# Kernel tuning notes

Measured on AMD Instinct MI355X. Metric: run time of the kernel, lower is better.

Reference implementation:

```python
import jax, jax.numpy as jnp
import numpy as np

MAX_DISP = 4  # matches init_kwargs


def setup_inputs() -> dict:
    key = jax.random.key(0)
    k1, k2 = jax.random.split(key)
    x_1 = jax.random.normal(k1, (8, 64, 256, 256), dtype=jnp.float32)
    x_2 = jax.random.normal(k2, (8, 64, 256, 256), dtype=jnp.float32)
    return {"x_1": x_1, "x_2": x_2}


def reference(x_1, x_2):
    md = MAX_DISP
    B, C, H, W = x_1.shape
    # zero-pad x_2 spatially by max_disp on all sides
    x2p = jnp.pad(x_2, ((0, 0), (0, 0), (md, md), (md, md)))
    D = 2 * md + 1
    # row-major over (dx, dy), matching torch.meshgrid(indexing='ij')
    outs = [
        jnp.mean(x_1 * jax.lax.dynamic_slice(x2p, (0, 0, dx, dy), (B, C, H, W)),
                 axis=1, keepdims=True)
        for dx in range(D) for dy in range(D)
    ]
    return jnp.concatenate(outs, axis=1)  # [B, D*D, H, W]
```

## Files before the change

### kernel.cpp

```cpp
#include <hip/hip_runtime.h>


namespace {
constexpr int kB = 8;
constexpr int kC = 64;
constexpr int kH = 256;
constexpr int kW = 256;
constexpr int kD = 9;
constexpr int kMD = 4;
}

__global__ __launch_bounds__(64) void corr_kernel(
    const float* __restrict__ x1, const float* __restrict__ x2,
    float* __restrict__ out) {
  const int bx = blockIdx.x;
  const int dx = bx % kD;
  const int h  = (bx / kD) % kH;
  const int b  = bx / (kD * kH);
  const int row = h + dx - kMD;
  const int w0  = (int)threadIdx.x * 4;

  float acc[kD][4];
#pragma unroll
  for (int dy = 0; dy < kD; ++dy)
#pragma unroll
    for (int j = 0; j < 4; ++j) acc[dy][j] = 0.0f;

  if (row >= 0 && row < kH) {
    const float* p1 = x1 + ((size_t)(b * kC) * kH + h) * kW + w0;
    const float* p2 = x2 + ((size_t)(b * kC) * kH + row) * kW + w0;
    const bool hasL = (w0 >= 4);
    const bool hasR = (w0 + 7 < kW);
    for (int c = 0; c < kC; ++c) {
      const float4 a  = *reinterpret_cast<const float4*>(p1);
      const float4 tB = *reinterpret_cast<const float4*>(p2);
      float4 tA = make_float4(0.f, 0.f, 0.f, 0.f);
      float4 tC = make_float4(0.f, 0.f, 0.f, 0.f);
      if (hasL) tA = *reinterpret_cast<const float4*>(p2 - 4);
      if (hasR) tC = *reinterpret_cast<const float4*>(p2 + 4);

      const float av[4] = {a.x, a.y, a.z, a.w};
      const float t[12] = {tA.x, tA.y, tA.z, tA.w,
                           tB.x, tB.y, tB.z, tB.w,
                           tC.x, tC.y, tC.z, tC.w};
#pragma unroll
      for (int dy = 0; dy < kD; ++dy)
#pragma unroll
        for (int j = 0; j < 4; ++j)
          acc[dy][j] = fmaf(av[j], t[dy + j], acc[dy][j]);

      p1 += kH * kW;
      p2 += kH * kW;
    }
  }

  const float inv = 1.0f / (float)kC;
  float* po = out + (((size_t)b * (kD * kD) + dx * kD) * kH + h) * kW + w0;
#pragma unroll
  for (int dy = 0; dy < kD; ++dy) {
    float4 o = make_float4(acc[dy][0] * inv, acc[dy][1] * inv,
                           acc[dy][2] * inv, acc[dy][3] * inv);
    *reinterpret_cast<float4*>(po) = o;
    po += (size_t)kH * kW;
  }
}

extern "C" void kernel_launch(void* const* d_in, const int* in_sizes, int n_in,
                              void* d_out, int out_size, void* d_ws, size_t ws_size,
                              hipStream_t stream) {
  const float* x1 = (const float*)d_in[0];
  const float* x2 = (const float*)d_in[1];
  float* out = (float*)d_out;
  const int grid = kB * kH * kD;
  corr_kernel<<<grid, 64, 0, stream>>>(x1, x2, out);
}
```

Measured before the change: 225.4 us.

## Stage row pairs in double-buffered LDS and share x2 rows across displacements

Each block now handles two output rows for all nine vertical displacements. Per channel it stages 2 x1 rows and 10 x2 rows into a swizzled, double-buffered shared-memory tile, with the next channel's global loads overlapped against compute. This replaces the old scheme, where every (row, dx) block re-read x1 and x2 from global memory. Each thread computes 8 output columns instead of 4 to raise register reuse. The cost is a barrier per channel, a 24KB LDS footprint, 72 accumulators per thread, and a much smaller grid of 1024 blocks.

```diff
diff --git a/kernel.cpp b/kernel.cpp
--- a/kernel.cpp
+++ b/kernel.cpp
@@ -7,60 +7,132 @@
 constexpr int kH = 256;
 constexpr int kW = 256;
 constexpr int kD = 9;
-constexpr int kMD = 4;
+constexpr int kCS = kH * kW;
+constexpr int kRows = 12;
+constexpr int kBufDw = kRows * kW;
 }
 
-__global__ __launch_bounds__(64) void corr_kernel(
+__device__ __forceinline__ int swz(int b) { return b ^ ((b >> 3) & 7); }
+
+__global__ __launch_bounds__(576) void corr_kernel(
     const float* __restrict__ x1, const float* __restrict__ x2,
     float* __restrict__ out) {
-  const int bx = blockIdx.x;
-  const int dx = bx % kD;
-  const int h  = (bx / kD) % kH;
-  const int b  = bx / (kD * kH);
-  const int row = h + dx - kMD;
-  const int w0  = (int)threadIdx.x * 4;
+  __shared__ float lds[2 * kBufDw];
 
-  float acc[kD][4];
+  const int bb = blockIdx.x & 7;
+  const int hp = blockIdx.x >> 3;
+  const int tid = (int)threadIdx.x;
+  const int wv = tid >> 6;
+  const int lane = tid & 63;
+  const int half = lane >> 5;
+  const int lh = lane & 31;
+  const int h = 2 * hp + half;
+  const int w0 = lh * 8;
+
+  const bool hasL = (lh > 0);
+  const bool hasR = (lh < 31);
+  const float4 z = make_float4(0.f, 0.f, 0.f, 0.f);
+
+  const size_t chanBase = (size_t)(bb * kC) * kH;
+
+  const int r0s = tid >> 6, b0s = tid & 63;
+  const float* src0;
+  bool v0;
+  if (r0s < 2) {
+    v0 = true;
+    src0 = x1 + (chanBase + (size_t)(2 * hp + r0s)) * kW + b0s * 4;
+  } else {
+    const int rr = 2 * hp + r0s - 6;
+    v0 = (rr >= 0 && rr < kH);
+    src0 = x2 + (chanBase + (size_t)(v0 ? rr : 0)) * kW + b0s * 4;
+  }
+  const int w0i = r0s * kW + swz(b0s) * 4;
+
+  const bool have1 = (tid < 192);
+  const int r1s = (576 + tid) >> 6, b1s = (576 + tid) & 63;
+  const float* src1 = x2;
+  bool v1 = false;
+  int w1i = 0;
+  if (have1) {
+    const int rr = 2 * hp + r1s - 6;
+    v1 = (rr >= 0 && rr < kH);
+    src1 = x2 + (chanBase + (size_t)(v1 ? rr : 0)) * kW + b1s * 4;
+    w1i = r1s * kW + swz(b1s) * 4;
+  }
+
+  const int a0i = half * kW + swz(2 * lh) * 4;
+  const int a1i = half * kW + swz(2 * lh + 1) * 4;
+  const int Rr = (2 + half + wv) * kW;
+  const int t0i = Rr + swz((2 * lh - 1) & 63) * 4;
+  const int t1i = Rr + swz(2 * lh) * 4;
+  const int t2i = Rr + swz(2 * lh + 1) * 4;
+  const int t3i = Rr + swz((2 * lh + 2) & 63) * 4;
+
+  float acc[kD][8];
 #pragma unroll
   for (int dy = 0; dy < kD; ++dy)
 #pragma unroll
-    for (int j = 0; j < 4; ++j) acc[dy][j] = 0.0f;
+    for (int j = 0; j < 8; ++j) acc[dy][j] = 0.0f;
 
-  if (row >= 0 && row < kH) {
-    const float* p1 = x1 + ((size_t)(b * kC) * kH + h) * kW + w0;
-    const float* p2 = x2 + ((size_t)(b * kC) * kH + row) * kW + w0;
-    const bool hasL = (w0 >= 4);
-    const bool hasR = (w0 + 7 < kW);
-    for (int c = 0; c < kC; ++c) {
-      const float4 a  = *reinterpret_cast<const float4*>(p1);
-      const float4 tB = *reinterpret_cast<const float4*>(p2);
-      float4 tA = make_float4(0.f, 0.f, 0.f, 0.f);
-      float4 tC = make_float4(0.f, 0.f, 0.f, 0.f);
-      if (hasL) tA = *reinterpret_cast<const float4*>(p2 - 4);
-      if (hasR) tC = *reinterpret_cast<const float4*>(p2 + 4);
+  {
+    const float4 g0 = v0 ? *reinterpret_cast<const float4*>(src0) : z;
+    *reinterpret_cast<float4*>(&lds[w0i]) = g0;
+    if (have1) {
+      const float4 g1 = v1 ? *reinterpret_cast<const float4*>(src1) : z;
+      *reinterpret_cast<float4*>(&lds[w1i]) = g1;
+    }
+    src0 += kCS;
+    src1 += kCS;
+  }
+  __syncthreads();
 
-      const float av[4] = {a.x, a.y, a.z, a.w};
-      const float t[12] = {tA.x, tA.y, tA.z, tA.w,
-                           tB.x, tB.y, tB.z, tB.w,
-                           tC.x, tC.y, tC.z, tC.w};
+#pragma unroll 2
+  for (int c = 0; c < kC; ++c) {
+    const int bo = (c & 1) ? kBufDw : 0;
+    const int bo2 = (c & 1) ? 0 : kBufDw;
+    const bool more = (c + 1 < kC);
+
+    float4 n0 = z, n1 = z;
+    if (more) {
+      n0 = v0 ? *reinterpret_cast<const float4*>(src0) : z;
+      if (have1) n1 = v1 ? *reinterpret_cast<const float4*>(src1) : z;
+      src0 += kCS;
+      src1 += kCS;
+    }
+
+    const float4 A0 = *reinterpret_cast<const float4*>(&lds[bo + a0i]);
+    const float4 A1 = *reinterpret_cast<const float4*>(&lds[bo + a1i]);
+    const float4 T0 = hasL ? *reinterpret_cast<const float4*>(&lds[bo + t0i]) : z;
+    const float4 T1 = *reinterpret_cast<const float4*>(&lds[bo + t1i]);
+    const float4 T2 = *reinterpret_cast<const float4*>(&lds[bo + t2i]);
+    const float4 T3 = hasR ? *reinterpret_cast<const float4*>(&lds[bo + t3i]) : z;
+
+    const float av[8] = {A0.x, A0.y, A0.z, A0.w, A1.x, A1.y, A1.z, A1.w};
+    const float t[16] = {T0.x, T0.y, T0.z, T0.w, T1.x, T1.y, T1.z, T1.w,
+                         T2.x, T2.y, T2.z, T2.w, T3.x, T3.y, T3.z, T3.w};
 #pragma unroll
-      for (int dy = 0; dy < kD; ++dy)
+    for (int dy = 0; dy < kD; ++dy)
 #pragma unroll
-        for (int j = 0; j < 4; ++j)
-          acc[dy][j] = fmaf(av[j], t[dy + j], acc[dy][j]);
+      for (int j = 0; j < 8; ++j)
+        acc[dy][j] = fmaf(av[j], t[dy + j], acc[dy][j]);
 
-      p1 += kH * kW;
-      p2 += kH * kW;
+    if (more) {
+      *reinterpret_cast<float4*>(&lds[bo2 + w0i]) = n0;
+      if (have1) *reinterpret_cast<float4*>(&lds[bo2 + w1i]) = n1;
+      __syncthreads();
     }
   }
 
   const float inv = 1.0f / (float)kC;
-  float* po = out + (((size_t)b * (kD * kD) + dx * kD) * kH + h) * kW + w0;
+  float* po = out + (((size_t)bb * (kD * kD) + wv * kD) * kH + h) * kW + w0;
 #pragma unroll
   for (int dy = 0; dy < kD; ++dy) {
-    float4 o = make_float4(acc[dy][0] * inv, acc[dy][1] * inv,
-                           acc[dy][2] * inv, acc[dy][3] * inv);
-    *reinterpret_cast<float4*>(po) = o;
+    const float4 o0 = make_float4(acc[dy][0] * inv, acc[dy][1] * inv,
+                                  acc[dy][2] * inv, acc[dy][3] * inv);
+    const float4 o1 = make_float4(acc[dy][4] * inv, acc[dy][5] * inv,
+                                  acc[dy][6] * inv, acc[dy][7] * inv);
+    *reinterpret_cast<float4*>(po) = o0;
+    *reinterpret_cast<float4*>(po + 4) = o1;
     po += (size_t)kH * kW;
   }
 }
@@ -71,6 +143,6 @@
   const float* x1 = (const float*)d_in[0];
   const float* x2 = (const float*)d_in[1];
   float* out = (float*)d_out;
-  const int grid = kB * kH * kD;
-  corr_kernel<<<grid, 64, 0, stream>>>(x1, x2, out);
+  const int grid = kB * (kH / 2);
+  corr_kernel<<<grid, 576, 0, stream>>>(x1, x2, out);
 }
```

Result: slower. 476.9 us (+111.5%).
